# Kernel tuning notes

Measured on AMD Instinct MI355X. Metric: run time of the kernel, lower is better.

## Reference

```python
import jax, jax.numpy as jnp
import numpy as np

N_IN = 262144
N_OUT = 262144
K = 27          # 3^3 kernel offsets
M = 131072      # pairs per kernel offset
C_IN = 64
C_OUT = 64
EPS = 1e-5
NEG_SLOPE = 0.01


def setup_inputs() -> dict:
    key = jax.random.key(0)
    k1, k2, k3, k4 = jax.random.split(key, 4)
    feats = jax.random.normal(k1, (N_IN, C_IN), dtype=jnp.float32)
    W = jax.random.normal(k2, (K, C_IN, C_OUT), dtype=jnp.float32) * (1.0 / np.sqrt(C_IN * K))
    gamma = jnp.ones((C_OUT,), dtype=jnp.float32)
    beta = jnp.zeros((C_OUT,), dtype=jnp.float32)
    in_map = jax.random.randint(k3, (K, M), 0, N_IN, dtype=jnp.int32)
    out_map = jax.random.randint(k4, (K, M), 0, N_OUT, dtype=jnp.int32)
    return {"feats": feats, "W": W, "gamma": gamma, "beta": beta,
            "in_map": in_map, "out_map": out_map, "num_out": N_OUT}


def sparse_conv(feats, W, in_map, out_map, num_out):
    # gather-matmul-scatter over K kernel offsets, accumulated via scan
    out0 = jnp.zeros((num_out, W.shape[2]), dtype=feats.dtype)

    def body(acc, xs):
        w, im, om = xs                       # w: [Cin,Cout], im/om: [M]
        contrib = feats[im] @ w              # [M, Cout]
        return acc.at[om].add(contrib), None

    out, _ = jax.lax.scan(body, out0, (W, in_map, out_map))
    return out


def reference(feats, W, gamma, beta, in_map, out_map, num_out):
    out = sparse_conv(feats, W, in_map, out_map, num_out)   # [N_out, Cout]
    # BatchNorm (training mode, biased variance over the point dim)
    mean = out.mean(axis=0)
    var = out.var(axis=0)
    y = (out - mean) * jax.lax.rsqrt(var + EPS) * gamma + beta
    # LeakyReLU, negative_slope = 0.01
    return jnp.where(y >= 0, y, NEG_SLOPE * y)
```

## Files before the change

### kernel.cpp

```cpp
#include <hip/hip_runtime.h>

#define N_IN   262144
#define N_OUT  262144
#define KOFF   27
#define MPAIR  131072
#define C      64
#define EPS    1e-5f
#define NEG_SLOPE 0.01f

__global__ __launch_bounds__(256) void conv_kernel(
    const float* __restrict__ feats,
    const float* __restrict__ W,
    const int*   __restrict__ in_map,
    const int*   __restrict__ out_map,
    float*       __restrict__ out)
{
    const int k    = blockIdx.y;
    const int lane = threadIdx.x & 63;
    const int wave = threadIdx.x >> 6;

    __shared__ float4 fr4[4][2][16];

    float wreg[C];
    const float* Wk = W + (size_t)k * C * C;
    #pragma unroll
    for (int i = 0; i < C; ++i) wreg[i] = Wk[i * C + lane];

    const int pair_base = (blockIdx.x * 4 + wave) * 64;
    const int my_pair   = pair_base + lane;
    const int my_im = in_map[(size_t)k * MPAIR + my_pair];
    const int my_om = out_map[(size_t)k * MPAIR + my_pair];

    int im0 = __builtin_amdgcn_readlane(my_im, 0);
    float fcur = feats[(size_t)im0 * C + lane];

    for (int p = 0; p < 64; ++p) {
        const int om  = __builtin_amdgcn_readlane(my_om, p);
        const int buf = p & 1;

        ((float*)&fr4[wave][buf][0])[lane] = fcur;

        if (p < 63) {
            int imn = __builtin_amdgcn_readlane(my_im, p + 1);
            fcur = feats[(size_t)imn * C + lane];
        }

        float acc = 0.f;
        #pragma unroll
        for (int j = 0; j < 16; ++j) {
            float4 f = fr4[wave][buf][j];
            acc = fmaf(f.x, wreg[4*j+0], acc);
            acc = fmaf(f.y, wreg[4*j+1], acc);
            acc = fmaf(f.z, wreg[4*j+2], acc);
            acc = fmaf(f.w, wreg[4*j+3], acc);
        }

        unsafeAtomicAdd(&out[(size_t)om * C + lane], acc);
    }
}

__global__ __launch_bounds__(256) void stats_kernel(
    const float* __restrict__ out, float* __restrict__ stats)
{
    __shared__ float4 s_sum[256], s_sq[256];
    const int col4 = threadIdx.x & 15;
    const int rowg = threadIdx.x >> 4;

    float4 s = make_float4(0.f, 0.f, 0.f, 0.f);
    float4 q = make_float4(0.f, 0.f, 0.f, 0.f);
    for (int row = blockIdx.x * 16 + rowg; row < N_OUT; row += gridDim.x * 16) {
        float4 v = *(const float4*)(out + (size_t)row * C + col4 * 4);
        s.x += v.x; s.y += v.y; s.z += v.z; s.w += v.w;
        q.x = fmaf(v.x, v.x, q.x); q.y = fmaf(v.y, v.y, q.y);
        q.z = fmaf(v.z, v.z, q.z); q.w = fmaf(v.w, v.w, q.w);
    }
    s_sum[threadIdx.x] = s; s_sq[threadIdx.x] = q;
    __syncthreads();

    if (threadIdx.x < 16) {
        float4 ts = make_float4(0.f, 0.f, 0.f, 0.f);
        float4 tq = make_float4(0.f, 0.f, 0.f, 0.f);
        for (int j = 0; j < 16; ++j) {
            float4 a = s_sum[j * 16 + threadIdx.x];
            float4 b = s_sq [j * 16 + threadIdx.x];
            ts.x += a.x; ts.y += a.y; ts.z += a.z; ts.w += a.w;
            tq.x += b.x; tq.y += b.y; tq.z += b.z; tq.w += b.w;
        }
        const int c0 = threadIdx.x * 4;
        unsafeAtomicAdd(&stats[c0 + 0], ts.x);
        unsafeAtomicAdd(&stats[c0 + 1], ts.y);
        unsafeAtomicAdd(&stats[c0 + 2], ts.z);
        unsafeAtomicAdd(&stats[c0 + 3], ts.w);
        unsafeAtomicAdd(&stats[64 + c0 + 0], tq.x);
        unsafeAtomicAdd(&stats[64 + c0 + 1], tq.y);
        unsafeAtomicAdd(&stats[64 + c0 + 2], tq.z);
        unsafeAtomicAdd(&stats[64 + c0 + 3], tq.w);
    }
}

__global__ __launch_bounds__(256) void bn_kernel(
    float* __restrict__ out,
    const float* __restrict__ stats,
    const float* __restrict__ gamma,
    const float* __restrict__ beta)
{
    __shared__ __align__(16) float s_scale[C];
    __shared__ __align__(16) float s_shift[C];
    if (threadIdx.x < C) {
        const float inv_n = 1.0f / (float)N_OUT;
        float mean = stats[threadIdx.x] * inv_n;
        float var  = stats[C + threadIdx.x] * inv_n - mean * mean;
        float sc   = gamma[threadIdx.x] * rsqrtf(var + EPS);
        s_scale[threadIdx.x] = sc;
        s_shift[threadIdx.x] = beta[threadIdx.x] - mean * sc;
    }
    __syncthreads();

    const int col4 = threadIdx.x & 15;
    const int rowg = threadIdx.x >> 4;
    const float4 sc4 = *(const float4*)&s_scale[col4 * 4];
    const float4 sh4 = *(const float4*)&s_shift[col4 * 4];

    for (int row = blockIdx.x * 16 + rowg; row < N_OUT; row += gridDim.x * 16) {
        float4* p = (float4*)(out + (size_t)row * C + col4 * 4);
        float4 v = *p;
        v.x = fmaf(v.x, sc4.x, sh4.x);
        v.y = fmaf(v.y, sc4.y, sh4.y);
        v.z = fmaf(v.z, sc4.z, sh4.z);
        v.w = fmaf(v.w, sc4.w, sh4.w);
        v.x = v.x >= 0.f ? v.x : NEG_SLOPE * v.x;
        v.y = v.y >= 0.f ? v.y : NEG_SLOPE * v.y;
        v.z = v.z >= 0.f ? v.z : NEG_SLOPE * v.z;
        v.w = v.w >= 0.f ? v.w : NEG_SLOPE * v.w;
        *p = v;
    }
}

extern "C" void kernel_launch(void* const* d_in, const int* in_sizes, int n_in,
                              void* d_out, int out_size, void* d_ws, size_t ws_size,
                              hipStream_t stream) {
    const float* feats  = (const float*)d_in[0];
    const float* W      = (const float*)d_in[1];
    const float* gamma  = (const float*)d_in[2];
    const float* beta   = (const float*)d_in[3];
    const int*  in_map  = (const int*)d_in[4];
    const int*  out_map = (const int*)d_in[5];

    float* out   = (float*)d_out;
    float* stats = (float*)d_ws;

    hipMemsetAsync(out, 0, (size_t)N_OUT * C * sizeof(float), stream);
    hipMemsetAsync(stats, 0, 2 * C * sizeof(float), stream);

    dim3 cgrid(MPAIR / 256, KOFF);
    conv_kernel<<<cgrid, 256, 0, stream>>>(feats, W, in_map, out_map, out);
    stats_kernel<<<256, 256, 0, stream>>>(out, stats);
    bn_kernel<<<512, 256, 0, stream>>>(out, stats, gamma, beta);
}
```

Measured before the change: 943.9 us.

## Bucket pairs by output block and accumulate in shared memory with fused stats

Replaces the per-offset gather-matmul-global-atomic conv with a counting sort (histogram, three-stage scan, scatter) that buckets pairs by output row block and kernel offset. A gather kernel then accumulates each 128-row output block in LDS with shared atomics, writes it once, and folds the BatchNorm sum/sumsq reduction into the same pass. This removes the global atomics and the output memset, and drops the separate stats kernel. The cost is several extra sort kernels plus a sorted-pair buffer. Each wave now walks a variable-length bucket serially, and only 2048 blocks run, so load balance and parallelism may suffer.

```diff
diff --git a/kernel.cpp b/kernel.cpp
--- a/kernel.cpp
+++ b/kernel.cpp
@@ -4,105 +4,169 @@
 #define N_OUT  262144
 #define KOFF   27
 #define MPAIR  131072
+#define NTOT   (KOFF * MPAIR)
 #define C      64
+#define RPB    128
+#define NBLK   (N_OUT / RPB)
+#define NKEY   (NBLK * KOFF)
+#define SCANB  (NKEY / 256)
 #define EPS    1e-5f
 #define NEG_SLOPE 0.01f
 
-__global__ __launch_bounds__(256) void conv_kernel(
-    const float* __restrict__ feats,
-    const float* __restrict__ W,
-    const int*   __restrict__ in_map,
-    const int*   __restrict__ out_map,
-    float*       __restrict__ out)
-{
-    const int k    = blockIdx.y;
-    const int lane = threadIdx.x & 63;
-    const int wave = threadIdx.x >> 6;
-
-    __shared__ float4 fr4[4][2][16];
-
-    float wreg[C];
-    const float* Wk = W + (size_t)k * C * C;
+typedef unsigned int u32;
+
+__global__ __launch_bounds__(256) void hist_kernel(
+    const int* __restrict__ out_map, u32* __restrict__ counts)
+{
+    int i = blockIdx.x * 256 + threadIdx.x;
+    int k = i >> 17;
+    int om = out_map[i];
+    atomicAdd(&counts[(u32)(om >> 7) * KOFF + (u32)k], 1u);
+}
+
+__global__ __launch_bounds__(256) void scan1_kernel(
+    const u32* __restrict__ counts, u32* __restrict__ partial, u32* __restrict__ bsums)
+{
+    __shared__ u32 sh[256];
+    int t = threadIdx.x, g = blockIdx.x * 256 + t;
+    u32 v = counts[g];
+    sh[t] = v; __syncthreads();
+    for (int off = 1; off < 256; off <<= 1) {
+        u32 a = (t >= off) ? sh[t - off] : 0u;
+        __syncthreads(); sh[t] += a; __syncthreads();
+    }
+    partial[g] = sh[t] - v;
+    if (t == 255) bsums[blockIdx.x] = sh[t];
+}
+
+__global__ __launch_bounds__(256) void scan2_kernel(u32* __restrict__ bsums)
+{
+    __shared__ u32 sh[256];
+    int t = threadIdx.x;
+    u32 v = (t < SCANB) ? bsums[t] : 0u;
+    sh[t] = v; __syncthreads();
+    for (int off = 1; off < 256; off <<= 1) {
+        u32 a = (t >= off) ? sh[t - off] : 0u;
+        __syncthreads(); sh[t] += a; __syncthreads();
+    }
+    if (t < SCANB) bsums[t] = sh[t] - v;
+}
+
+__global__ __launch_bounds__(256) void scan3_kernel(
+    const u32* __restrict__ partial, const u32* __restrict__ bsums,
+    u32* __restrict__ offsets, u32* __restrict__ cursor)
+{
+    int g = blockIdx.x * 256 + threadIdx.x;
+    u32 o = partial[g] + bsums[blockIdx.x];
+    offsets[g] = o; cursor[g] = o;
+    if (g == 0) offsets[NKEY] = NTOT;
+}
+
+__global__ __launch_bounds__(256) void scatter_kernel(
+    const int* __restrict__ in_map, const int* __restrict__ out_map,
+    u32* __restrict__ cursor, u32* __restrict__ sorted)
+{
+    int i = blockIdx.x * 256 + threadIdx.x;
+    int k = i >> 17;
+    int om = out_map[i];
+    u32 im = (u32)in_map[i];
+    u32 key = (u32)(om >> 7) * KOFF + (u32)k;
+    u32 pos = atomicAdd(&cursor[key], 1u);
+    sorted[pos] = ((u32)(om & 127) << 23) | ((u32)k << 18) | im;
+}
+
+__global__ __launch_bounds__(256, 4) void gather_kernel(
+    const float* __restrict__ feats, const float* __restrict__ W,
+    const u32* __restrict__ offsets, const u32* __restrict__ sorted,
+    float* __restrict__ out, float* __restrict__ stats)
+{
+    __shared__ float accs[RPB][C];
+    __shared__ float frow[4][C];
+    const int t = threadIdx.x, lane = t & 63, wave = t >> 6;
+    const int b = blockIdx.x;
+
+    {
+        float4* az = (float4*)&accs[0][0];
+        #pragma unroll
+        for (int j = 0; j < RPB * C / 4 / 256; ++j)
+            az[j * 256 + t] = make_float4(0.f, 0.f, 0.f, 0.f);
+    }
+    __syncthreads();
+
+    for (int kk = wave; kk < KOFF; kk += 4) {
+        const u32 start = offsets[b * KOFF + kk];
+        const u32 end   = offsets[b * KOFF + kk + 1];
+        if (start == end) continue;
+
+        float wcol[C];
+        const float* Wk = W + kk * C * C;
+        #pragma unroll
+        for (int i = 0; i < C; ++i) wcol[i] = Wk[i * C + lane];
+
+        u32 ent = sorted[start];
+        float fcur = feats[(size_t)(ent & 0x3FFFFu) * C + lane];
+
+        for (u32 e = start; e < end; ++e) {
+            const int lrow = (int)(ent >> 23);
+            frow[wave][lane] = fcur;
+            if (e + 1 < end) {
+                ent  = sorted[e + 1];
+                fcur = feats[(size_t)(ent & 0x3FFFFu) * C + lane];
+            }
+            float a = 0.f;
+            const float4* f4 = (const float4*)&frow[wave][0];
+            #pragma unroll
+            for (int j = 0; j < 16; ++j) {
+                float4 f = f4[j];
+                a = fmaf(f.x, wcol[4 * j + 0], a);
+                a = fmaf(f.y, wcol[4 * j + 1], a);
+                a = fmaf(f.z, wcol[4 * j + 2], a);
+                a = fmaf(f.w, wcol[4 * j + 3], a);
+            }
+            atomicAdd(&accs[lrow][lane], a);
+        }
+    }
+    __syncthreads();
+
+    const int col4 = t & 15, rowg = t >> 4;
+    float4 s4 = make_float4(0.f, 0.f, 0.f, 0.f);
+    float4 q4 = make_float4(0.f, 0.f, 0.f, 0.f);
+    float4* outv = (float4*)out;
     #pragma unroll
-    for (int i = 0; i < C; ++i) wreg[i] = Wk[i * C + lane];
-
-    const int pair_base = (blockIdx.x * 4 + wave) * 64;
-    const int my_pair   = pair_base + lane;
-    const int my_im = in_map[(size_t)k * MPAIR + my_pair];
-    const int my_om = out_map[(size_t)k * MPAIR + my_pair];
-
-    int im0 = __builtin_amdgcn_readlane(my_im, 0);
-    float fcur = feats[(size_t)im0 * C + lane];
-
-    for (int p = 0; p < 64; ++p) {
-        const int om  = __builtin_amdgcn_readlane(my_om, p);
-        const int buf = p & 1;
-
-        ((float*)&fr4[wave][buf][0])[lane] = fcur;
-
-        if (p < 63) {
-            int imn = __builtin_amdgcn_readlane(my_im, p + 1);
-            fcur = feats[(size_t)imn * C + lane];
-        }
-
-        float acc = 0.f;
-        #pragma unroll
-        for (int j = 0; j < 16; ++j) {
-            float4 f = fr4[wave][buf][j];
-            acc = fmaf(f.x, wreg[4*j+0], acc);
-            acc = fmaf(f.y, wreg[4*j+1], acc);
-            acc = fmaf(f.z, wreg[4*j+2], acc);
-            acc = fmaf(f.w, wreg[4*j+3], acc);
-        }
-
-        unsafeAtomicAdd(&out[(size_t)om * C + lane], acc);
-    }
-}
-
-__global__ __launch_bounds__(256) void stats_kernel(
-    const float* __restrict__ out, float* __restrict__ stats)
-{
-    __shared__ float4 s_sum[256], s_sq[256];
-    const int col4 = threadIdx.x & 15;
-    const int rowg = threadIdx.x >> 4;
-
-    float4 s = make_float4(0.f, 0.f, 0.f, 0.f);
-    float4 q = make_float4(0.f, 0.f, 0.f, 0.f);
-    for (int row = blockIdx.x * 16 + rowg; row < N_OUT; row += gridDim.x * 16) {
-        float4 v = *(const float4*)(out + (size_t)row * C + col4 * 4);
-        s.x += v.x; s.y += v.y; s.z += v.z; s.w += v.w;
-        q.x = fmaf(v.x, v.x, q.x); q.y = fmaf(v.y, v.y, q.y);
-        q.z = fmaf(v.z, v.z, q.z); q.w = fmaf(v.w, v.w, q.w);
-    }
-    s_sum[threadIdx.x] = s; s_sq[threadIdx.x] = q;
-    __syncthreads();
-
-    if (threadIdx.x < 16) {
+    for (int r = rowg; r < RPB; r += 16) {
+        float4 v = *((const float4*)&accs[r][0] + col4);
+        outv[(size_t)(b * RPB + r) * 16 + col4] = v;
+        s4.x += v.x; s4.y += v.y; s4.z += v.z; s4.w += v.w;
+        q4.x = fmaf(v.x, v.x, q4.x); q4.y = fmaf(v.y, v.y, q4.y);
+        q4.z = fmaf(v.z, v.z, q4.z); q4.w = fmaf(v.w, v.w, q4.w);
+    }
+    __syncthreads();
+    float4* sc = (float4*)&accs[0][0];
+    sc[t] = s4; sc[256 + t] = q4;
+    __syncthreads();
+    if (t < 16) {
         float4 ts = make_float4(0.f, 0.f, 0.f, 0.f);
         float4 tq = make_float4(0.f, 0.f, 0.f, 0.f);
         for (int j = 0; j < 16; ++j) {
-            float4 a = s_sum[j * 16 + threadIdx.x];
-            float4 b = s_sq [j * 16 + threadIdx.x];
+            float4 a = sc[j * 16 + t], bq = sc[256 + j * 16 + t];
             ts.x += a.x; ts.y += a.y; ts.z += a.z; ts.w += a.w;
-            tq.x += b.x; tq.y += b.y; tq.z += b.z; tq.w += b.w;
+            tq.x += bq.x; tq.y += bq.y; tq.z += bq.z; tq.w += bq.w;
         }
-        const int c0 = threadIdx.x * 4;
+        const int c0 = t * 4;
         unsafeAtomicAdd(&stats[c0 + 0], ts.x);
         unsafeAtomicAdd(&stats[c0 + 1], ts.y);
         unsafeAtomicAdd(&stats[c0 + 2], ts.z);
         unsafeAtomicAdd(&stats[c0 + 3], ts.w);
-        unsafeAtomicAdd(&stats[64 + c0 + 0], tq.x);
-        unsafeAtomicAdd(&stats[64 + c0 + 1], tq.y);
-        unsafeAtomicAdd(&stats[64 + c0 + 2], tq.z);
-        unsafeAtomicAdd(&stats[64 + c0 + 3], tq.w);
+        unsafeAtomicAdd(&stats[C + c0 + 0], tq.x);
+        unsafeAtomicAdd(&stats[C + c0 + 1], tq.y);
+        unsafeAtomicAdd(&stats[C + c0 + 2], tq.z);
+        unsafeAtomicAdd(&stats[C + c0 + 3], tq.w);
     }
 }
 
 __global__ __launch_bounds__(256) void bn_kernel(
-    float* __restrict__ out,
-    const float* __restrict__ stats,
-    const float* __restrict__ gamma,
-    const float* __restrict__ beta)
+    float* __restrict__ out, const float* __restrict__ stats,
+    const float* __restrict__ gamma, const float* __restrict__ beta)
 {
     __shared__ __align__(16) float s_scale[C];
     __shared__ __align__(16) float s_shift[C];
@@ -146,14 +210,24 @@
     const int*  in_map  = (const int*)d_in[4];
     const int*  out_map = (const int*)d_in[5];
 
-    float* out   = (float*)d_out;
-    float* stats = (float*)d_ws;
-
-    hipMemsetAsync(out, 0, (size_t)N_OUT * C * sizeof(float), stream);
+    float* out = (float*)d_out;
+
+    u32* counts  = (u32*)d_ws;
+    u32* partial = counts  + NKEY;
+    u32* bsums   = partial + NKEY;
+    u32* offsets = bsums   + 256;
+    u32* cursor  = offsets + NKEY + 16;
+    u32* sorted  = cursor  + NKEY;
+    float* stats = (float*)(sorted + NTOT);
+
+    hipMemsetAsync(counts, 0, NKEY * sizeof(u32), stream);
     hipMemsetAsync(stats, 0, 2 * C * sizeof(float), stream);
 
-    dim3 cgrid(MPAIR / 256, KOFF);
-    conv_kernel<<<cgrid, 256, 0, stream>>>(feats, W, in_map, out_map, out);
-    stats_kernel<<<256, 256, 0, stream>>>(out, stats);
-    bn_kernel<<<512, 256, 0, stream>>>(out, stats, gamma, beta);
-}
+    hist_kernel   <<<NTOT / 256, 256, 0, stream>>>(out_map, counts);
+    scan1_kernel  <<<SCANB,      256, 0, stream>>>(counts, partial, bsums);
+    scan2_kernel  <<<1,          256, 0, stream>>>(bsums);
+    scan3_kernel  <<<SCANB,      256, 0, stream>>>(partial, bsums, offsets, cursor);
+    scatter_kernel<<<NTOT / 256, 256, 0, stream>>>(in_map, out_map, cursor, sorted);
+    gather_kernel <<<NBLK,       256, 0, stream>>>(feats, W, offsets, sorted, out, stats);
+    bn_kernel     <<<512,        256, 0, stream>>>(out, stats, gamma, beta);
+}
```

New measurement: 2.140 ms. +126.7%, slower.
